# Optimization experiments

Hardware: AMD Instinct MI355X
Metric: run time of the kernel (lower is better)

## Reference

```python
import jax, jax.numpy as jnp
import numpy as np
from jax import lax

S_DIM = 64
A_DIM = 32
HIDDEN = 30
BATCH = 524288
BUDGET = 90.0   # cp constraint: sum(y) == 90
U_VAL = 10.0    # per-dim action upper bound a_bound
N_BISECT = 60


def project_capped_simplex(z, u, s):
    """argmin_y ||y - z||^2  s.t. sum(y)=s, 0<=y<=u.
    Solution y = clip(z - lam, 0, u) with scalar dual lam found by bisection,
    followed by differentiable Newton steps so implicit gradients are exact.
    z: [B, D], u: [D]."""
    zs = lax.stop_gradient(z)
    lo = jnp.min(zs - u, axis=-1)  # sum = sum(u) >= s
    hi = jnp.max(zs, axis=-1)      # sum = 0 <= s

    def body(i, lohi):
        lo, hi = lohi
        mid = 0.5 * (lo + hi)
        gm = jnp.sum(jnp.clip(zs - mid[..., None], 0.0, u), axis=-1) - s
        lo = jnp.where(gm > 0, mid, lo)
        hi = jnp.where(gm > 0, hi, mid)
        return (lo, hi)

    lo, hi = lax.fori_loop(0, N_BISECT, body, (lo, hi))
    lam = 0.5 * (lo + hi)  # already stop-gradient (derived from zs)

    # two differentiable semismooth-Newton refinements -> correct implicit VJP
    for _ in range(2):
        d = z - lam[..., None]
        y = jnp.clip(d, 0.0, u)
        g = jnp.sum(y, axis=-1) - s
        active = ((d > 0) & (d < u)).astype(z.dtype)
        gp = -jnp.sum(active, axis=-1)
        lam = lam - g / jnp.where(gp == 0, -1.0, gp)

    return jnp.clip(z - lam[..., None], 0.0, u)


def setup_inputs() -> dict:
    key = jax.random.key(0)
    ks = jax.random.split(key, 8)
    x = jax.random.normal(ks[0], (BATCH, S_DIM), dtype=jnp.float32)
    W1 = 0.1 * jax.random.normal(ks[1], (HIDDEN, S_DIM), dtype=jnp.float32)
    b1 = 0.1 * jax.random.normal(ks[2], (HIDDEN,), dtype=jnp.float32)
    W2 = 0.1 * jax.random.normal(ks[3], (A_DIM, HIDDEN), dtype=jnp.float32)
    b2 = 0.1 * jax.random.normal(ks[4], (A_DIM,), dtype=jnp.float32)
    Wopt = 0.001 * jax.random.normal(ks[5], (A_DIM, A_DIM), dtype=jnp.float32)
    bopt = 0.001 * jax.random.normal(ks[6], (A_DIM,), dtype=jnp.float32)
    u = U_VAL * jnp.ones((A_DIM,), dtype=jnp.float32)
    return {"x": x, "W1": W1, "b1": b1, "W2": W2, "b2": b2,
            "Wopt": Wopt, "bopt": bopt, "u": u}


def reference(x, W1, b1, W2, b2, Wopt, bopt, u):
    # fc1 -> relu -> out -> tanh
    h = jax.nn.relu(x @ W1.T + b1)            # [B, 30]
    t = jnp.tanh(h @ W2.T + b2)               # [B, A_DIM]
    # OptLayer QP: min ||Wopt @ t - bopt - y||^2 s.t. sum(y)=90, 0<=y<=u
    z = t @ Wopt.T - bopt                     # [B, A_DIM]
    y = project_capped_simplex(z, u, BUDGET)  # [B, A_DIM]
    return y
```

## Files before the change

kernel.cpp:

```cpp
#include <hip/hip_runtime.h>
#include <hip/hip_bf16.h>


typedef __attribute__((ext_vector_type(8))) short bf16x8;
typedef __attribute__((ext_vector_type(4))) float f32x4;

constexpr int SDIM = 64, HID = 30, ADIM = 32, BATCH = 524288;
constexpr float BUDGET = 90.0f;
constexpr int NBIS = 16;
constexpr int TILES = BATCH / 16;

static __device__ __forceinline__ short f2bf(float f) {
    __hip_bfloat16 h = __float2bfloat16(f);
    return (short)__builtin_bit_cast(unsigned short, h);
}

static __device__ __forceinline__ float fast_exp2(float a) {
#if __has_builtin(__builtin_amdgcn_exp2f)
    return __builtin_amdgcn_exp2f(a);
#else
    return exp2f(a);
#endif
}
static __device__ __forceinline__ float fast_rcp(float a) {
#if __has_builtin(__builtin_amdgcn_rcpf)
    return __builtin_amdgcn_rcpf(a);
#else
    return 1.0f / a;
#endif
}
static __device__ __forceinline__ float tanh_fast(float a) {
    const float e = fast_exp2(a * 2.8853900817779268f);
    return 1.0f - 2.0f * fast_rcp(e + 1.0f);
}

static __device__ __forceinline__ int swz(int r, int cidx) {
    return r * 32 + ((((cidx >> 2) ^ (r & 7))) << 2) + (cidx & 3);
}

__global__ __launch_bounds__(256) void anet_mfma(
    const float* __restrict__ x,
    const float* __restrict__ W1, const float* __restrict__ b1,
    const float* __restrict__ W2, const float* __restrict__ b2,
    const float* __restrict__ Wopt, const float* __restrict__ bopt,
    const float* __restrict__ u,
    float* __restrict__ out)
{
    __shared__ float smem[4 * 512];
    const int lane = threadIdx.x & 63;
    const int wid  = threadIdx.x >> 6;
    float* sm = &smem[wid * 512];

    const int c = lane & 15;
    const int g = lane >> 4;

    auto loadB = [&](const float* W, int stride, int ncol, int kvalid,
                     int nt, int k0) -> bf16x8 {
        const int col = c + 16 * nt;
        const bool okc = (col < ncol);
        const float* p = W + (okc ? col : 0) * stride + k0;
        bf16x8 b;
#pragma unroll
        for (int j = 0; j < 8; ++j) {
            const int kk = k0 + j;
            const int jj = (kk < kvalid) ? j : (kvalid - 1 - k0);
            float v = p[jj];
            v = (okc && kk < kvalid) ? v : 0.0f;
            b[j] = f2bf(v);
        }
        return b;
    };
    bf16x8 B1[2][2], B2[2], B3[2];
    B1[0][0] = loadB(W1, 64, HID, 64, 0, g * 8);
    B1[1][0] = loadB(W1, 64, HID, 64, 0, 32 + g * 8);
    B1[0][1] = loadB(W1, 64, HID, 64, 1, g * 8);
    B1[1][1] = loadB(W1, 64, HID, 64, 1, 32 + g * 8);
    B2[0]    = loadB(W2, HID, ADIM, HID, 0, g * 8);
    B2[1]    = loadB(W2, HID, ADIM, HID, 1, g * 8);
    B3[0]    = loadB(Wopt, ADIM, ADIM, ADIM, 0, g * 8);
    B3[1]    = loadB(Wopt, ADIM, ADIM, ADIM, 1, g * 8);

    const float b1c0 = b1[c];
    const float b1c1 = (c + 16 < HID) ? b1[c + 16] : 0.0f;
    const float b2c0 = b2[c],   b2c1 = b2[c + 16];
    const float boc0 = bopt[c], boc1 = bopt[c + 16];

    const int rrow = lane >> 2;
    const int dseg = lane & 3;
    float u8[8];
    {
        const float4 ua = *reinterpret_cast<const float4*>(u + dseg * 8);
        const float4 ub = *reinterpret_cast<const float4*>(u + dseg * 8 + 4);
        u8[0]=ua.x; u8[1]=ua.y; u8[2]=ua.z; u8[3]=ua.w;
        u8[4]=ub.x; u8[5]=ub.y; u8[6]=ub.z; u8[7]=ub.w;
    }

    auto read_afrag = [&]() -> bf16x8 {
        const float4 lo4 = *reinterpret_cast<const float4*>(
            &sm[c * 32 + (((2 * g) ^ (c & 7)) << 2)]);
        const float4 hi4 = *reinterpret_cast<const float4*>(
            &sm[c * 32 + (((2 * g + 1) ^ (c & 7)) << 2)]);
        bf16x8 a;
        a[0]=f2bf(lo4.x); a[1]=f2bf(lo4.y); a[2]=f2bf(lo4.z); a[3]=f2bf(lo4.w);
        a[4]=f2bf(hi4.x); a[5]=f2bf(hi4.y); a[6]=f2bf(hi4.z); a[7]=f2bf(hi4.w);
        return a;
    };

    const f32x4 zero4 = {0.0f, 0.0f, 0.0f, 0.0f};
    const int gw = blockIdx.x * 4 + wid;
    const int nw = gridDim.x * 4;

    for (int tl = gw; tl < TILES; tl += nw) {
        const float* xb = x + (tl * 16 + c) * SDIM + g * 8;
        const float4 x00 = *reinterpret_cast<const float4*>(xb);
        const float4 x01 = *reinterpret_cast<const float4*>(xb + 4);
        const float4 x10 = *reinterpret_cast<const float4*>(xb + 32);
        const float4 x11 = *reinterpret_cast<const float4*>(xb + 36);
        bf16x8 xa0, xa1;
        xa0[0]=f2bf(x00.x); xa0[1]=f2bf(x00.y); xa0[2]=f2bf(x00.z); xa0[3]=f2bf(x00.w);
        xa0[4]=f2bf(x01.x); xa0[5]=f2bf(x01.y); xa0[6]=f2bf(x01.z); xa0[7]=f2bf(x01.w);
        xa1[0]=f2bf(x10.x); xa1[1]=f2bf(x10.y); xa1[2]=f2bf(x10.z); xa1[3]=f2bf(x10.w);
        xa1[4]=f2bf(x11.x); xa1[5]=f2bf(x11.y); xa1[6]=f2bf(x11.z); xa1[7]=f2bf(x11.w);

        f32x4 acc0 = __builtin_amdgcn_mfma_f32_16x16x32_bf16(xa0, B1[0][0], zero4, 0, 0, 0);
        acc0       = __builtin_amdgcn_mfma_f32_16x16x32_bf16(xa1, B1[1][0], acc0, 0, 0, 0);
        f32x4 acc1 = __builtin_amdgcn_mfma_f32_16x16x32_bf16(xa0, B1[0][1], zero4, 0, 0, 0);
        acc1       = __builtin_amdgcn_mfma_f32_16x16x32_bf16(xa1, B1[1][1], acc1, 0, 0, 0);
#pragma unroll
        for (int q = 0; q < 4; ++q) {
            const int r = 4 * g + q;
            sm[swz(r, c)]      = fmaxf(acc0[q] + b1c0, 0.0f);
            sm[swz(r, c + 16)] = fmaxf(acc1[q] + b1c1, 0.0f);
        }
        asm volatile("s_waitcnt lgkmcnt(0)" ::: "memory");

        const bf16x8 haf = read_afrag();
        acc0 = __builtin_amdgcn_mfma_f32_16x16x32_bf16(haf, B2[0], zero4, 0, 0, 0);
        acc1 = __builtin_amdgcn_mfma_f32_16x16x32_bf16(haf, B2[1], zero4, 0, 0, 0);
#pragma unroll
        for (int q = 0; q < 4; ++q) {
            const int r = 4 * g + q;
            sm[swz(r, c)]      = tanh_fast(acc0[q] + b2c0);
            sm[swz(r, c + 16)] = tanh_fast(acc1[q] + b2c1);
        }
        asm volatile("s_waitcnt lgkmcnt(0)" ::: "memory");

        const bf16x8 taf = read_afrag();
        acc0 = __builtin_amdgcn_mfma_f32_16x16x32_bf16(taf, B3[0], zero4, 0, 0, 0);
        acc1 = __builtin_amdgcn_mfma_f32_16x16x32_bf16(taf, B3[1], zero4, 0, 0, 0);
#pragma unroll
        for (int q = 0; q < 4; ++q) {
            const int r = 4 * g + q;
            sm[swz(r, c)]      = acc0[q] - boc0;
            sm[swz(r, c + 16)] = acc1[q] - boc1;
        }
        asm volatile("s_waitcnt lgkmcnt(0)" ::: "memory");

        const float4 za = *reinterpret_cast<const float4*>(
            &sm[rrow * 32 + (((2 * dseg) ^ (rrow & 7)) << 2)]);
        const float4 zb = *reinterpret_cast<const float4*>(
            &sm[rrow * 32 + (((2 * dseg + 1) ^ (rrow & 7)) << 2)]);
        float z8[8] = {za.x, za.y, za.z, za.w, zb.x, zb.y, zb.z, zb.w};

        float mx = z8[0], mn = z8[0] - u8[0];
#pragma unroll
        for (int j = 1; j < 8; ++j) {
            mx = fmaxf(mx, z8[j]);
            mn = fminf(mn, z8[j] - u8[j]);
        }
        mx = fmaxf(mx, __shfl_xor(mx, 1)); mx = fmaxf(mx, __shfl_xor(mx, 2));
        mn = fminf(mn, __shfl_xor(mn, 1)); mn = fminf(mn, __shfl_xor(mn, 2));
        float lo = mn, hi = mx;

#pragma unroll 1
        for (int it = 0; it < NBIS; ++it) {
            const float mid = 0.5f * (lo + hi);
            float s0 = fminf(fmaxf(z8[0] - mid, 0.0f), u8[0])
                     + fminf(fmaxf(z8[1] - mid, 0.0f), u8[1]);
            float s1 = fminf(fmaxf(z8[2] - mid, 0.0f), u8[2])
                     + fminf(fmaxf(z8[3] - mid, 0.0f), u8[3]);
            float s2 = fminf(fmaxf(z8[4] - mid, 0.0f), u8[4])
                     + fminf(fmaxf(z8[5] - mid, 0.0f), u8[5]);
            float s3 = fminf(fmaxf(z8[6] - mid, 0.0f), u8[6])
                     + fminf(fmaxf(z8[7] - mid, 0.0f), u8[7]);
            float s = (s0 + s1) + (s2 + s3);
            s += __shfl_xor(s, 1);
            s += __shfl_xor(s, 2);
            const bool pos = (s > BUDGET);
            lo = pos ? mid : lo;
            hi = pos ? hi : mid;
        }
        const float lam = 0.5f * (lo + hi);

        float4 y0, y1;
        y0.x = fminf(fmaxf(z8[0] - lam, 0.0f), u8[0]);
        y0.y = fminf(fmaxf(z8[1] - lam, 0.0f), u8[1]);
        y0.z = fminf(fmaxf(z8[2] - lam, 0.0f), u8[2]);
        y0.w = fminf(fmaxf(z8[3] - lam, 0.0f), u8[3]);
        y1.x = fminf(fmaxf(z8[4] - lam, 0.0f), u8[4]);
        y1.y = fminf(fmaxf(z8[5] - lam, 0.0f), u8[5]);
        y1.z = fminf(fmaxf(z8[6] - lam, 0.0f), u8[6]);
        y1.w = fminf(fmaxf(z8[7] - lam, 0.0f), u8[7]);
        float* ob = out + (tl * 16 + rrow) * ADIM + dseg * 8;
        *reinterpret_cast<float4*>(ob)     = y0;
        *reinterpret_cast<float4*>(ob + 4) = y1;
    }
}

extern "C" void kernel_launch(void* const* d_in, const int* in_sizes, int n_in,
                              void* d_out, int out_size, void* d_ws, size_t ws_size,
                              hipStream_t stream)
{
    const float* x    = (const float*)d_in[0];
    const float* W1   = (const float*)d_in[1];
    const float* b1   = (const float*)d_in[2];
    const float* W2   = (const float*)d_in[3];
    const float* b2   = (const float*)d_in[4];
    const float* Wopt = (const float*)d_in[5];
    const float* bopt = (const float*)d_in[6];
    const float* u    = (const float*)d_in[7];
    float* out = (float*)d_out;

    const int threads = 256;
    const int blocks  = 1024;
    anet_mfma<<<blocks, threads, 0, stream>>>(x, W1, b1, W2, b2, Wopt, bopt, u, out);
}
```

Measured before the change: 237.6 us.

## Add closed-form projection fast path, DPP reductions, and prefetch x tiles

Computes the unconstrained dual lambda = (sum z - budget)/32 and skips bisection when every row in the wave has all entries strictly inside (0,u) at that lambda. Quad reductions switch from shuffles to DPP moves. The tile loop becomes a fixed 4-tile unrolled loop that prefetches the next tile's x, with twice as many blocks launched. The fixed TPW=4 plus 2048 blocks assumes exact coverage of all tiles, which matches BATCH (32768 tiles), and the fast path depends on the data keeping rows interior.

```diff
diff --git a/kernel.cpp b/kernel.cpp
--- a/kernel.cpp
+++ b/kernel.cpp
@@ -33,6 +33,18 @@
     const float e = fast_exp2(a * 2.8853900817779268f);
     return 1.0f - 2.0f * fast_rcp(e + 1.0f);
 }
+
+template <int CTRL, int XOR>
+static __device__ __forceinline__ float qp_mov(float v) {
+#if __has_builtin(__builtin_amdgcn_mov_dpp)
+    return __builtin_bit_cast(float,
+        __builtin_amdgcn_mov_dpp(__builtin_bit_cast(int, v), CTRL, 0xF, 0xF, true));
+#else
+    return __shfl_xor(v, XOR, 4);
+#endif
+}
+static __device__ __forceinline__ float qp_x1(float v) { return qp_mov<0xB1, 1>(v); }
+static __device__ __forceinline__ float qp_x2(float v) { return qp_mov<0x4E, 2>(v); }
 
 static __device__ __forceinline__ int swz(int r, int cidx) {
     return r * 32 + ((((cidx >> 2) ^ (r & 7))) << 2) + (cidx & 3);
@@ -109,18 +121,34 @@
     const f32x4 zero4 = {0.0f, 0.0f, 0.0f, 0.0f};
     const int gw = blockIdx.x * 4 + wid;
     const int nw = gridDim.x * 4;
-
-    for (int tl = gw; tl < TILES; tl += nw) {
-        const float* xb = x + (tl * 16 + c) * SDIM + g * 8;
-        const float4 x00 = *reinterpret_cast<const float4*>(xb);
-        const float4 x01 = *reinterpret_cast<const float4*>(xb + 4);
-        const float4 x10 = *reinterpret_cast<const float4*>(xb + 32);
-        const float4 x11 = *reinterpret_cast<const float4*>(xb + 36);
+    constexpr int TPW = 4;
+
+    float4 nx0, nx1, nx2, nx3;
+    {
+        const float* xb = x + (gw * 16 + c) * SDIM + g * 8;
+        nx0 = *reinterpret_cast<const float4*>(xb);
+        nx1 = *reinterpret_cast<const float4*>(xb + 4);
+        nx2 = *reinterpret_cast<const float4*>(xb + 32);
+        nx3 = *reinterpret_cast<const float4*>(xb + 36);
+    }
+
+#pragma unroll
+    for (int k = 0; k < TPW; ++k) {
+        const int tl = gw + k * nw;
+        const float4 cx0 = nx0, cx1 = nx1, cx2 = nx2, cx3 = nx3;
+        if (k + 1 < TPW) {
+            const float* xb = x + ((gw + (k + 1) * nw) * 16 + c) * SDIM + g * 8;
+            nx0 = *reinterpret_cast<const float4*>(xb);
+            nx1 = *reinterpret_cast<const float4*>(xb + 4);
+            nx2 = *reinterpret_cast<const float4*>(xb + 32);
+            nx3 = *reinterpret_cast<const float4*>(xb + 36);
+        }
+
         bf16x8 xa0, xa1;
-        xa0[0]=f2bf(x00.x); xa0[1]=f2bf(x00.y); xa0[2]=f2bf(x00.z); xa0[3]=f2bf(x00.w);
-        xa0[4]=f2bf(x01.x); xa0[5]=f2bf(x01.y); xa0[6]=f2bf(x01.z); xa0[7]=f2bf(x01.w);
-        xa1[0]=f2bf(x10.x); xa1[1]=f2bf(x10.y); xa1[2]=f2bf(x10.z); xa1[3]=f2bf(x10.w);
-        xa1[4]=f2bf(x11.x); xa1[5]=f2bf(x11.y); xa1[6]=f2bf(x11.z); xa1[7]=f2bf(x11.w);
+        xa0[0]=f2bf(cx0.x); xa0[1]=f2bf(cx0.y); xa0[2]=f2bf(cx0.z); xa0[3]=f2bf(cx0.w);
+        xa0[4]=f2bf(cx1.x); xa0[5]=f2bf(cx1.y); xa0[6]=f2bf(cx1.z); xa0[7]=f2bf(cx1.w);
+        xa1[0]=f2bf(cx2.x); xa1[1]=f2bf(cx2.y); xa1[2]=f2bf(cx2.z); xa1[3]=f2bf(cx2.w);
+        xa1[4]=f2bf(cx3.x); xa1[5]=f2bf(cx3.y); xa1[6]=f2bf(cx3.z); xa1[7]=f2bf(cx3.w);
 
         f32x4 acc0 = __builtin_amdgcn_mfma_f32_16x16x32_bf16(xa0, B1[0][0], zero4, 0, 0, 0);
         acc0       = __builtin_amdgcn_mfma_f32_16x16x32_bf16(xa1, B1[1][0], acc0, 0, 0, 0);
@@ -160,37 +188,48 @@
             &sm[rrow * 32 + (((2 * dseg) ^ (rrow & 7)) << 2)]);
         const float4 zb = *reinterpret_cast<const float4*>(
             &sm[rrow * 32 + (((2 * dseg + 1) ^ (rrow & 7)) << 2)]);
-        float z8[8] = {za.x, za.y, za.z, za.w, zb.x, zb.y, zb.z, zb.w};
-
-        float mx = z8[0], mn = z8[0] - u8[0];
-#pragma unroll
-        for (int j = 1; j < 8; ++j) {
-            mx = fmaxf(mx, z8[j]);
-            mn = fminf(mn, z8[j] - u8[j]);
-        }
-        mx = fmaxf(mx, __shfl_xor(mx, 1)); mx = fmaxf(mx, __shfl_xor(mx, 2));
-        mn = fminf(mn, __shfl_xor(mn, 1)); mn = fminf(mn, __shfl_xor(mn, 2));
-        float lo = mn, hi = mx;
-
+        const float z8[8] = {za.x, za.y, za.z, za.w, zb.x, zb.y, zb.z, zb.w};
+
+        float ps = ((z8[0] + z8[1]) + (z8[2] + z8[3]))
+                 + ((z8[4] + z8[5]) + (z8[6] + z8[7]));
+        float pmnz = fminf(fminf(fminf(z8[0], z8[1]), fminf(z8[2], z8[3])),
+                           fminf(fminf(z8[4], z8[5]), fminf(z8[6], z8[7])));
+        float d0 = z8[0]-u8[0], d1 = z8[1]-u8[1], d2 = z8[2]-u8[2], d3 = z8[3]-u8[3];
+        float d4 = z8[4]-u8[4], d5 = z8[5]-u8[5], d6 = z8[6]-u8[6], d7 = z8[7]-u8[7];
+        float pmxzu = fmaxf(fmaxf(fmaxf(d0, d1), fmaxf(d2, d3)),
+                            fmaxf(fmaxf(d4, d5), fmaxf(d6, d7)));
+        ps += qp_x1(ps);  ps += qp_x2(ps);
+        pmnz  = fminf(pmnz,  qp_x1(pmnz));  pmnz  = fminf(pmnz,  qp_x2(pmnz));
+        pmxzu = fmaxf(pmxzu, qp_x1(pmxzu)); pmxzu = fmaxf(pmxzu, qp_x2(pmxzu));
+        const float lam_unc = (ps - BUDGET) * (1.0f / 32.0f);
+        const bool ok = (pmxzu <= lam_unc) && (lam_unc <= pmnz);
+
+        float lam;
+        if (__all(ok)) {
+            lam = lam_unc;
+        } else {
+            float lo = fminf(fminf(fminf(d0, d1), fminf(d2, d3)),
+                             fminf(fminf(d4, d5), fminf(d6, d7)));
+            float hi = fmaxf(fmaxf(fmaxf(z8[0], z8[1]), fmaxf(z8[2], z8[3])),
+                             fmaxf(fmaxf(z8[4], z8[5]), fmaxf(z8[6], z8[7])));
+            lo = fminf(lo, qp_x1(lo)); lo = fminf(lo, qp_x2(lo));
+            hi = fmaxf(hi, qp_x1(hi)); hi = fmaxf(hi, qp_x2(hi));
 #pragma unroll 1
-        for (int it = 0; it < NBIS; ++it) {
-            const float mid = 0.5f * (lo + hi);
-            float s0 = fminf(fmaxf(z8[0] - mid, 0.0f), u8[0])
-                     + fminf(fmaxf(z8[1] - mid, 0.0f), u8[1]);
-            float s1 = fminf(fmaxf(z8[2] - mid, 0.0f), u8[2])
-                     + fminf(fmaxf(z8[3] - mid, 0.0f), u8[3]);
-            float s2 = fminf(fmaxf(z8[4] - mid, 0.0f), u8[4])
-                     + fminf(fmaxf(z8[5] - mid, 0.0f), u8[5]);
-            float s3 = fminf(fmaxf(z8[6] - mid, 0.0f), u8[6])
-                     + fminf(fmaxf(z8[7] - mid, 0.0f), u8[7]);
-            float s = (s0 + s1) + (s2 + s3);
-            s += __shfl_xor(s, 1);
-            s += __shfl_xor(s, 2);
-            const bool pos = (s > BUDGET);
-            lo = pos ? mid : lo;
-            hi = pos ? hi : mid;
-        }
-        const float lam = 0.5f * (lo + hi);
+            for (int it = 0; it < NBIS; ++it) {
+                const float mid = 0.5f * (lo + hi);
+                float s = -BUDGET * 0.25f;
+#pragma unroll
+                for (int i = 0; i < 8; ++i)
+                    s += fminf(fmaxf(z8[i] - mid, 0.0f), u8[i]);
+                s += qp_x1(s);
+                s += qp_x2(s);
+                const bool pos = (s > 0.0f);
+                lo = pos ? mid : lo;
+                hi = pos ? hi : mid;
+            }
+            const float lam_b = 0.5f * (lo + hi);
+            lam = ok ? lam_unc : lam_b;
+        }
 
         float4 y0, y1;
         y0.x = fminf(fmaxf(z8[0] - lam, 0.0f), u8[0]);
@@ -222,6 +261,6 @@
     float* out = (float*)d_out;
 
     const int threads = 256;
-    const int blocks  = 1024;
+    const int blocks  = 2048;
     anet_mfma<<<blocks, threads, 0, stream>>>(x, W1, b1, W2, b2, Wopt, bopt, u, out);
 }
```

After: 232.8 us. -2.0%, faster.
